# Optimization experiments

Hardware: AMD Instinct MI355X
Metric: run time of the kernel (lower is better)

Reference implementation:

```python
import jax, jax.numpy as jnp
import numpy as np

B, G, N, C = 8, 16, 1024, 256


def setup_inputs() -> dict:
    key = jax.random.key(0)
    k1, k2, k3, k4, k5 = jax.random.split(key, 5)
    x = jax.random.normal(k1, (B, G, N, C), dtype=jnp.float32)
    vs = jax.random.normal(k2, (B, G, 1, N, 3), dtype=jnp.float32)
    s = 1.0 / np.sqrt(C)
    W_fc = jax.random.normal(k3, (C, C), dtype=jnp.float32) * s   # nn.Linear weight [out,in]
    b_fc = jax.random.normal(k4, (C,), dtype=jnp.float32) * s
    W_vn = jax.random.normal(k5, (C, C), dtype=jnp.float32) * s   # VNLinear weight [out,in], no bias
    return {"x": x, "vs": vs, "W_fc": W_fc, "b_fc": b_fc, "W_vn": W_vn}


def reference(x, vs, W_fc, b_fc, W_vn):
    # q = fc(x): [B,G,N,C]
    q = jnp.einsum('bgnc,oc->bgno', x, W_fc) + b_fc
    # softmax over the point dim N (torch dim=2)
    atten = jax.nn.softmax(q, axis=2)
    xw = atten * x  # [B,G,N,C]
    # torch: expand to [B,G,C,N,3] * vs then sum over N.
    # Equivalent contraction without materializing the 5D tensor:
    v = jnp.squeeze(vs, axis=2)  # [B,G,N,3]
    out = jnp.einsum('bgnc,bgnd->bgcd', xw, v)  # [B,G,C,3]
    # VNLinear: bias-free linear over channel dim, shared across the 3 vector comps
    return jnp.einsum('bgcd,oc->bgod', out, W_vn)  # [B,G,C,3]
```

## Files before the change

### kernel.cpp

```cpp
#include <hip/hip_runtime.h>
#include <hip/hip_bf16.h>


#define NQ 1024
#define CQ 256
#define RT 64
#define XS 136
#define WB_OFF 131072

typedef __attribute__((ext_vector_type(8))) short bf16x8;
typedef __attribute__((ext_vector_type(4))) float f32x4;

__device__ __forceinline__ ushort2 pk2(float a, float b) {
    __hip_bfloat162 h = __float22bfloat162_rn(make_float2(a, b));
    ushort2 r;
    __builtin_memcpy(&r, &h, sizeof(r));
    return r;
}
__device__ __forceinline__ float bf2f(ushort h) {
    union { unsigned u; float f; } v; v.u = ((unsigned)h) << 16;
    return v.f;
}

__device__ __forceinline__ void bar_lgkm() {
    __builtin_amdgcn_sched_barrier(0);
    asm volatile("s_waitcnt lgkmcnt(0)" ::: "memory");
    __builtin_amdgcn_sched_barrier(0);
    __builtin_amdgcn_s_barrier();
    __builtin_amdgcn_sched_barrier(0);
}

__global__ __launch_bounds__(256)
void wfc_cvt(const float* __restrict__ Wfc, ushort* __restrict__ Wb) {
    const int i = blockIdx.x * 256 + threadIdx.x;
    float4 v = reinterpret_cast<const float4*>(Wfc)[i];
    ushort2 a0 = pk2(v.x, v.y), a1 = pk2(v.z, v.w);
    ushort4 pk = { a0.x, a0.y, a1.x, a1.y };
    reinterpret_cast<ushort4*>(Wb)[i] = pk;
}

__global__ __launch_bounds__(256, 4)
void attn_pool_partial(const float* __restrict__ x, const float* __restrict__ vs,
                       const ushort* __restrict__ Wb, float* __restrict__ ws) {
    __shared__ __align__(16) ushort xs0[RT * XS];
    __shared__ __align__(16) ushort xs1[RT * XS];
    __shared__ __align__(16) float  vsm[RT * 3];

    const int t = threadIdx.x;
    const int id = blockIdx.x;
    const int ch = (id >> 3) & 1;
    const int rest = (id & 7) | ((id >> 4) << 3);
    const int bg = rest >> 4;
    const int nt = rest & 15;
    const int n0 = nt * RT;
    const int c0 = ch * 128;

    const int w = t >> 6, lane = t & 63;
    const int quad = lane >> 4, l16 = lane & 15;
    const int cstrip = w * 32;

    const float* xb = x + (size_t)bg * NQ * CQ;
    const float* vb = vs + (size_t)bg * NQ * 3;

    const int srow = (t * 8) >> 5 >> 3;
    (void)srow;

    const int sidx_row[1] = {0}; (void)sidx_row;
    const bool vload = (t < 48);
    float4 vreg;
    if (vload) vreg = reinterpret_cast<const float4*>(vb + (size_t)n0 * 3)[t];

    const int kcA = (ch ^ 1) * 128, kcB = ch * 128;
    float4 LA[8], LB[8];
    #pragma unroll
    for (int p = 0; p < 8; ++p) {
        const int idx = p * 256 + t;
        const int row = idx >> 5, k4 = idx & 31;
        LA[p] = *reinterpret_cast<const float4*>(
            xb + (size_t)(n0 + row) * CQ + kcA + k4 * 4);
    }
    #pragma unroll
    for (int p = 0; p < 8; ++p) {
        const int idx = p * 256 + t;
        const int row = idx >> 5, k4 = idx & 31;
        LB[p] = *reinterpret_cast<const float4*>(
            xb + (size_t)(n0 + row) * CQ + kcB + k4 * 4);
    }

    #pragma unroll
    for (int p = 0; p < 8; ++p) {
        const int idx = p * 256 + t;
        const int row = idx >> 5, k4 = idx & 31;
        ushort2 a0 = pk2(LA[p].x, LA[p].y), a1 = pk2(LA[p].z, LA[p].w);
        ushort4 pk = { a0.x, a0.y, a1.x, a1.y };
        *reinterpret_cast<ushort4*>(&xs0[row * XS + k4 * 4]) = pk;
    }
    if (vload) reinterpret_cast<float4*>(vsm)[t] = vreg;

    bar_lgkm();

    f32x4 acc[4][2];
    #pragma unroll
    for (int m = 0; m < 4; ++m)
        #pragma unroll
        for (int ci = 0; ci < 2; ++ci) acc[m][ci] = (f32x4){0.f, 0.f, 0.f, 0.f};

    const int bcol0 = c0 + cstrip + l16;

    #pragma unroll
    for (int ks = 0; ks < 4; ++ks) {
        const int kk = ks * 32 + quad * 8;
        bf16x8 b0 = *reinterpret_cast<const bf16x8*>(Wb + (size_t)bcol0 * CQ + kcA + kk);
        bf16x8 b1 = *reinterpret_cast<const bf16x8*>(Wb + (size_t)(bcol0 + 16) * CQ + kcA + kk);
        #pragma unroll
        for (int m = 0; m < 4; ++m) {
            bf16x8 a = *reinterpret_cast<const bf16x8*>(&xs0[(m * 16 + l16) * XS + kk]);
            acc[m][0] = __builtin_amdgcn_mfma_f32_16x16x32_bf16(a, b0, acc[m][0], 0, 0, 0);
            acc[m][1] = __builtin_amdgcn_mfma_f32_16x16x32_bf16(a, b1, acc[m][1], 0, 0, 0);
        }
    }

    #pragma unroll
    for (int p = 0; p < 8; ++p) {
        const int idx = p * 256 + t;
        const int row = idx >> 5, k4 = idx & 31;
        ushort2 a0 = pk2(LB[p].x, LB[p].y), a1 = pk2(LB[p].z, LB[p].w);
        ushort4 pk = { a0.x, a0.y, a1.x, a1.y };
        *reinterpret_cast<ushort4*>(&xs1[row * XS + k4 * 4]) = pk;
    }

    bar_lgkm();

    #pragma unroll
    for (int ks = 0; ks < 4; ++ks) {
        const int kk = ks * 32 + quad * 8;
        bf16x8 b0 = *reinterpret_cast<const bf16x8*>(Wb + (size_t)bcol0 * CQ + kcB + kk);
        bf16x8 b1 = *reinterpret_cast<const bf16x8*>(Wb + (size_t)(bcol0 + 16) * CQ + kcB + kk);
        #pragma unroll
        for (int m = 0; m < 4; ++m) {
            bf16x8 a = *reinterpret_cast<const bf16x8*>(&xs1[(m * 16 + l16) * XS + kk]);
            acc[m][0] = __builtin_amdgcn_mfma_f32_16x16x32_bf16(a, b0, acc[m][0], 0, 0, 0);
            acc[m][1] = __builtin_amdgcn_mfma_f32_16x16x32_bf16(a, b1, acc[m][1], 0, 0, 0);
        }
    }

    float rZ[2] = {0.f, 0.f}, rS0[2] = {0.f, 0.f}, rS1[2] = {0.f, 0.f}, rS2[2] = {0.f, 0.f};
    #pragma unroll
    for (int m = 0; m < 4; ++m) {
        const int rbase = m * 16 + quad * 4;
        float v0[4], v1[4], v2[4];
        #pragma unroll
        for (int r = 0; r < 4; ++r) {
            v0[r] = vsm[(rbase + r) * 3 + 0];
            v1[r] = vsm[(rbase + r) * 3 + 1];
            v2[r] = vsm[(rbase + r) * 3 + 2];
        }
        #pragma unroll
        for (int ci = 0; ci < 2; ++ci) {
            const int xc = cstrip + ci * 16 + l16;
            #pragma unroll
            for (int r = 0; r < 4; ++r) {
                float e = __expf(acc[m][ci][r]);
                float xv = bf2f(xs1[(rbase + r) * XS + xc]);
                rZ[ci] += e;
                float p = e * xv;
                rS0[ci] = fmaf(p, v0[r], rS0[ci]);
                rS1[ci] = fmaf(p, v1[r], rS1[ci]);
                rS2[ci] = fmaf(p, v2[r], rS2[ci]);
            }
        }
    }

    #pragma unroll
    for (int ci = 0; ci < 2; ++ci) {
        float z = rZ[ci], s0 = rS0[ci], s1 = rS1[ci], s2 = rS2[ci];
        #pragma unroll
        for (int off = 16; off < 64; off <<= 1) {
            z  += __shfl_xor(z,  off);
            s0 += __shfl_xor(s0, off);
            s1 += __shfl_xor(s1, off);
            s2 += __shfl_xor(s2, off);
        }
        if (quad == 0) {
            const int col = c0 + cstrip + ci * 16 + l16;
            float* p = ws + ((size_t)bg * CQ + col) * 4;
            atomicAdd(&p[0], z);
            atomicAdd(&p[1], s0);
            atomicAdd(&p[2], s1);
            atomicAdd(&p[3], s2);
        }
    }
}

__global__ __launch_bounds__(256, 4)
void vn_linear(const float* __restrict__ ws, const float* __restrict__ Wvn,
               float* __restrict__ out) {
    __shared__ float Tsm[CQ][3];
    const int bg = blockIdx.x, t = threadIdx.x;
    {
        f32x4 z4 = *reinterpret_cast<const f32x4*>(ws + ((size_t)bg * CQ + t) * 4);
        float inv = 1.f / z4[0];
        Tsm[t][0] = z4[1] * inv;
        Tsm[t][1] = z4[2] * inv;
        Tsm[t][2] = z4[3] * inv;
    }
    __syncthreads();
    const float* wr = Wvn + (size_t)t * CQ;
    float a0 = 0.f, a1 = 0.f, a2 = 0.f;
    #pragma unroll
    for (int c = 0; c < CQ; c += 4) {
        float4 w4 = *reinterpret_cast<const float4*>(wr + c);
        a0 += w4.x * Tsm[c + 0][0] + w4.y * Tsm[c + 1][0]
            + w4.z * Tsm[c + 2][0] + w4.w * Tsm[c + 3][0];
        a1 += w4.x * Tsm[c + 0][1] + w4.y * Tsm[c + 1][1]
            + w4.z * Tsm[c + 2][1] + w4.w * Tsm[c + 3][1];
        a2 += w4.x * Tsm[c + 0][2] + w4.y * Tsm[c + 1][2]
            + w4.z * Tsm[c + 2][2] + w4.w * Tsm[c + 3][2];
    }
    float* op = out + ((size_t)bg * CQ + t) * 3;
    op[0] = a0; op[1] = a1; op[2] = a2;
}

extern "C" void kernel_launch(void* const* d_in, const int* in_sizes, int n_in,
                              void* d_out, int out_size, void* d_ws, size_t ws_size,
                              hipStream_t stream) {
    const float* x   = (const float*)d_in[0];
    const float* vs  = (const float*)d_in[1];
    const float* Wfc = (const float*)d_in[2];
    const float* Wvn = (const float*)d_in[4];
    float* out = (float*)d_out;
    float* ws  = (float*)d_ws;

    ushort* Wb = (ushort*)(ws + WB_OFF);

    (void)hipMemsetAsync(ws, 0, (size_t)128 * CQ * 4 * sizeof(float), stream);
    wfc_cvt<<<dim3(64), dim3(256), 0, stream>>>(Wfc, Wb);
    attn_pool_partial<<<dim3(4096), dim3(256), 0, stream>>>(x, vs, Wb, ws);
    vn_linear<<<dim3(128), dim3(256), 0, stream>>>(ws, Wvn, out);
}
```

Before: 230.3 us.

## Relayout bf16 W_fc into k-octet-major tiles and prefetch B fragments into registers

The converted bf16 W_fc is now stored k-octet-major (an [k/8][C][8] layout), so the 16-lane groups loading B fragments read contiguous 16-byte chunks instead of rows strided by 512 bytes. B fragments for both K halves are loaded into registers ahead of the MFMA loops, interleaved with the x loads, with sched_barriers fixing the issue order. The MFMA loops also raise wave priority with s_setprio. The aim is better coalescing of weight loads and keeping global-load latency off the MFMA chain, at the cost of more VGPRs held at 4 waves per SIMD.

```diff
diff --git a/kernel.cpp b/kernel.cpp
--- a/kernel.cpp
+++ b/kernel.cpp
@@ -31,17 +31,19 @@
 }
 
 __global__ __launch_bounds__(256)
-void wfc_cvt(const float* __restrict__ Wfc, ushort* __restrict__ Wb) {
+void wfc_cvt(const float* __restrict__ Wfc, ushort* __restrict__ WbT) {
     const int i = blockIdx.x * 256 + threadIdx.x;
-    float4 v = reinterpret_cast<const float4*>(Wfc)[i];
+    const int o = i >> 6;
+    const int k4 = (i & 63) * 4;
+    float4 v = *reinterpret_cast<const float4*>(Wfc + (size_t)o * CQ + k4);
     ushort2 a0 = pk2(v.x, v.y), a1 = pk2(v.z, v.w);
     ushort4 pk = { a0.x, a0.y, a1.x, a1.y };
-    reinterpret_cast<ushort4*>(Wb)[i] = pk;
+    *reinterpret_cast<ushort4*>(WbT + ((size_t)(k4 >> 3) * CQ + o) * 8 + (k4 & 7)) = pk;
 }
 
 __global__ __launch_bounds__(256, 4)
 void attn_pool_partial(const float* __restrict__ x, const float* __restrict__ vs,
-                       const ushort* __restrict__ Wb, float* __restrict__ ws) {
+                       const ushort* __restrict__ WbT, float* __restrict__ ws) {
     __shared__ __align__(16) ushort xs0[RT * XS];
     __shared__ __align__(16) ushort xs1[RT * XS];
     __shared__ __align__(16) float  vsm[RT * 3];
@@ -62,16 +64,15 @@
     const float* xb = x + (size_t)bg * NQ * CQ;
     const float* vb = vs + (size_t)bg * NQ * 3;
 
-    const int srow = (t * 8) >> 5 >> 3;
-    (void)srow;
-
-    const int sidx_row[1] = {0}; (void)sidx_row;
+    const int kcA = (ch ^ 1) * 128, kcB = ch * 128;
+    const int bcol0 = c0 + cstrip + l16;
+
     const bool vload = (t < 48);
     float4 vreg;
     if (vload) vreg = reinterpret_cast<const float4*>(vb + (size_t)n0 * 3)[t];
-
-    const int kcA = (ch ^ 1) * 128, kcB = ch * 128;
-    float4 LA[8], LB[8];
+    __builtin_amdgcn_sched_barrier(0);
+
+    float4 LA[8];
     #pragma unroll
     for (int p = 0; p < 8; ++p) {
         const int idx = p * 256 + t;
@@ -79,6 +80,21 @@
         LA[p] = *reinterpret_cast<const float4*>(
             xb + (size_t)(n0 + row) * CQ + kcA + k4 * 4);
     }
+    __builtin_amdgcn_sched_barrier(0);
+
+    bf16x8 BA0[4], BA1[4];
+    {
+        const ushort* WA = WbT + (size_t)(kcA >> 3) * (CQ * 8);
+        #pragma unroll
+        for (int ks = 0; ks < 4; ++ks) {
+            const size_t fo = (size_t)(ks * 4 + quad) * (CQ * 8);
+            BA0[ks] = *reinterpret_cast<const bf16x8*>(WA + fo + (size_t)bcol0 * 8);
+            BA1[ks] = *reinterpret_cast<const bf16x8*>(WA + fo + (size_t)(bcol0 + 16) * 8);
+        }
+    }
+    __builtin_amdgcn_sched_barrier(0);
+
+    float4 LB[8];
     #pragma unroll
     for (int p = 0; p < 8; ++p) {
         const int idx = p * 256 + t;
@@ -86,6 +102,7 @@
         LB[p] = *reinterpret_cast<const float4*>(
             xb + (size_t)(n0 + row) * CQ + kcB + k4 * 4);
     }
+    __builtin_amdgcn_sched_barrier(0);
 
     #pragma unroll
     for (int p = 0; p < 8; ++p) {
@@ -105,20 +122,31 @@
         #pragma unroll
         for (int ci = 0; ci < 2; ++ci) acc[m][ci] = (f32x4){0.f, 0.f, 0.f, 0.f};
 
-    const int bcol0 = c0 + cstrip + l16;
-
+    __builtin_amdgcn_s_setprio(1);
     #pragma unroll
     for (int ks = 0; ks < 4; ++ks) {
         const int kk = ks * 32 + quad * 8;
-        bf16x8 b0 = *reinterpret_cast<const bf16x8*>(Wb + (size_t)bcol0 * CQ + kcA + kk);
-        bf16x8 b1 = *reinterpret_cast<const bf16x8*>(Wb + (size_t)(bcol0 + 16) * CQ + kcA + kk);
         #pragma unroll
         for (int m = 0; m < 4; ++m) {
             bf16x8 a = *reinterpret_cast<const bf16x8*>(&xs0[(m * 16 + l16) * XS + kk]);
-            acc[m][0] = __builtin_amdgcn_mfma_f32_16x16x32_bf16(a, b0, acc[m][0], 0, 0, 0);
-            acc[m][1] = __builtin_amdgcn_mfma_f32_16x16x32_bf16(a, b1, acc[m][1], 0, 0, 0);
-        }
-    }
+            acc[m][0] = __builtin_amdgcn_mfma_f32_16x16x32_bf16(a, BA0[ks], acc[m][0], 0, 0, 0);
+            acc[m][1] = __builtin_amdgcn_mfma_f32_16x16x32_bf16(a, BA1[ks], acc[m][1], 0, 0, 0);
+        }
+    }
+    __builtin_amdgcn_s_setprio(0);
+    __builtin_amdgcn_sched_barrier(0);
+
+    bf16x8 BB0[4], BB1[4];
+    {
+        const ushort* WB = WbT + (size_t)(kcB >> 3) * (CQ * 8);
+        #pragma unroll
+        for (int ks = 0; ks < 4; ++ks) {
+            const size_t fo = (size_t)(ks * 4 + quad) * (CQ * 8);
+            BB0[ks] = *reinterpret_cast<const bf16x8*>(WB + fo + (size_t)bcol0 * 8);
+            BB1[ks] = *reinterpret_cast<const bf16x8*>(WB + fo + (size_t)(bcol0 + 16) * 8);
+        }
+    }
+    __builtin_amdgcn_sched_barrier(0);
 
     #pragma unroll
     for (int p = 0; p < 8; ++p) {
@@ -131,18 +159,18 @@
 
     bar_lgkm();
 
+    __builtin_amdgcn_s_setprio(1);
     #pragma unroll
     for (int ks = 0; ks < 4; ++ks) {
         const int kk = ks * 32 + quad * 8;
-        bf16x8 b0 = *reinterpret_cast<const bf16x8*>(Wb + (size_t)bcol0 * CQ + kcB + kk);
-        bf16x8 b1 = *reinterpret_cast<const bf16x8*>(Wb + (size_t)(bcol0 + 16) * CQ + kcB + kk);
         #pragma unroll
         for (int m = 0; m < 4; ++m) {
             bf16x8 a = *reinterpret_cast<const bf16x8*>(&xs1[(m * 16 + l16) * XS + kk]);
-            acc[m][0] = __builtin_amdgcn_mfma_f32_16x16x32_bf16(a, b0, acc[m][0], 0, 0, 0);
-            acc[m][1] = __builtin_amdgcn_mfma_f32_16x16x32_bf16(a, b1, acc[m][1], 0, 0, 0);
-        }
-    }
+            acc[m][0] = __builtin_amdgcn_mfma_f32_16x16x32_bf16(a, BB0[ks], acc[m][0], 0, 0, 0);
+            acc[m][1] = __builtin_amdgcn_mfma_f32_16x16x32_bf16(a, BB1[ks], acc[m][1], 0, 0, 0);
+        }
+    }
+    __builtin_amdgcn_s_setprio(0);
 
     float rZ[2] = {0.f, 0.f}, rS0[2] = {0.f, 0.f}, rS1[2] = {0.f, 0.f}, rS2[2] = {0.f, 0.f};
     #pragma unroll
@@ -231,10 +259,10 @@
     float* out = (float*)d_out;
     float* ws  = (float*)d_ws;
 
-    ushort* Wb = (ushort*)(ws + WB_OFF);
+    ushort* WbT = (ushort*)(ws + WB_OFF);
 
     (void)hipMemsetAsync(ws, 0, (size_t)128 * CQ * 4 * sizeof(float), stream);
-    wfc_cvt<<<dim3(64), dim3(256), 0, stream>>>(Wfc, Wb);
-    attn_pool_partial<<<dim3(4096), dim3(256), 0, stream>>>(x, vs, Wb, ws);
+    wfc_cvt<<<dim3(64), dim3(256), 0, stream>>>(Wfc, WbT);
+    attn_pool_partial<<<dim3(4096), dim3(256), 0, stream>>>(x, vs, WbT, ws);
     vn_linear<<<dim3(128), dim3(256), 0, stream>>>(ws, Wvn, out);
 }
```

Result: faster. 214.9 us (-6.7%).
